# Optimization experiments

Hardware: AMD Instinct MI355X
Metric: run time of the kernel (lower is better)

## Reference

```python
import jax, jax.numpy as jnp
import numpy as np

INPUT_DIM = 1024
HIDDEN_DIM = 1024
NUM_HEADS = 16
HEAD_DIM = HIDDEN_DIM // NUM_HEADS


def setup_inputs() -> dict:
    key = jax.random.key(0)
    ks = jax.random.split(key, 11)
    B, S = 2, 2048
    s_in = 1.0 / np.sqrt(INPUT_DIM)
    s_hid = 1.0 / np.sqrt(HIDDEN_DIM)
    return {
        "query": jax.random.normal(ks[0], (B, S, INPUT_DIM), jnp.float32),
        "key": jax.random.normal(ks[1], (B, S, INPUT_DIM), jnp.float32),
        "value": jax.random.normal(ks[2], (B, S, INPUT_DIM), jnp.float32),
        "Wq": jax.random.normal(ks[3], (INPUT_DIM, HIDDEN_DIM), jnp.float32) * s_in,
        "bq": jnp.zeros((HIDDEN_DIM,), jnp.float32),
        "Wk": jax.random.normal(ks[4], (INPUT_DIM, HEAD_DIM), jnp.float32) * s_in,
        "bk": jnp.zeros((HEAD_DIM,), jnp.float32),
        "Wv": jax.random.normal(ks[5], (INPUT_DIM, HEAD_DIM), jnp.float32) * s_in,
        "bv": jnp.zeros((HEAD_DIM,), jnp.float32),
        "Wo": jax.random.normal(ks[6], (HIDDEN_DIM, INPUT_DIM), jnp.float32) * s_hid,
        "bo": jnp.zeros((INPUT_DIM,), jnp.float32),
    }


def reference(query, key, value, Wq, bq, Wk, bk, Wv, bv, Wo, bo):
    B, S, _ = query.shape
    # projections
    q = query @ Wq + bq                       # [B,S,H*D]
    k = key @ Wk + bk                         # [B,S,D]  (single shared head)
    v = value @ Wv + bv                       # [B,S,D]
    q = q.reshape(B, S, NUM_HEADS, HEAD_DIM)  # [B,S,H,D]
    # MQA scores: shared K broadcast over query heads
    scores = jnp.einsum('bqhd,bkd->bhqk', q, k) / np.sqrt(HIDDEN_DIM)
    attn = jax.nn.softmax(scores, axis=-1)    # [B,H,Q,K]
    out = jnp.einsum('bhqk,bkd->bqhd', attn, v)  # [B,Q,H,D]
    out = out.reshape(B, S, HIDDEN_DIM)
    return out @ Wo + bo
```

## Files before the change

### kernel.cpp

```cpp
#include <hip/hip_runtime.h>


typedef unsigned int   u32;
typedef unsigned short u16;
typedef union { float4 v; float f[4]; } f4u;
typedef __attribute__((ext_vector_type(8)))  short frag16;
typedef __attribute__((ext_vector_type(4)))  float f32x4;
typedef __attribute__((ext_vector_type(16))) float f32x16;
typedef union { frag16 v; u32 w[4]; u16 e[8]; } bf8u;

static __device__ __forceinline__ u16 f2bf(float x) {
  union { float f; u32 u; } v; v.f = x;
  u32 r = v.u + 0x7fff + ((v.u >> 16) & 1);
  return (u16)(r >> 16);
}

static __device__ __forceinline__ u32 cvt_pk_bf16(float lo, float hi) {
  u32 r;
  asm("v_cvt_pk_bf16_f32 %0, %1, %2" : "=v"(r) : "v"(lo), "v"(hi));
  return r;
}

static __device__ void tcvt_tile(const float* __restrict__ src,
                                 u16* __restrict__ dst,
                                 int C, int ldT, int rt, int ct,
                                 float (*t)[65]) {
  const int r0 = rt * 64, c0 = ct * 64;
  const int tr  = threadIdx.x >> 4;
  const int tc4 = (threadIdx.x & 15) * 4;
#pragma unroll
  for (int i = 0; i < 4; ++i) {
    f4u v; v.v = *(const float4*)(src + (size_t)(r0 + tr + i * 16) * C + c0 + tc4);
    t[tr + i * 16][tc4 + 0] = v.f[0];
    t[tr + i * 16][tc4 + 1] = v.f[1];
    t[tr + i * 16][tc4 + 2] = v.f[2];
    t[tr + i * 16][tc4 + 3] = v.f[3];
  }
  __syncthreads();
#pragma unroll
  for (int i = 0; i < 4; ++i) {
    const int oc = tr + i * 16;
    ushort4 o;
    o.x = f2bf(t[tc4 + 0][oc]);
    o.y = f2bf(t[tc4 + 1][oc]);
    o.z = f2bf(t[tc4 + 2][oc]);
    o.w = f2bf(t[tc4 + 3][oc]);
    *(ushort4*)(dst + (size_t)(c0 + oc) * ldT + r0 + tc4) = o;
  }
}

__global__ __launch_bounds__(256)
void prep_w(const float* __restrict__ Wq, const float* __restrict__ Wo,
            const float* __restrict__ Wk, const float* __restrict__ Wv,
            u16* __restrict__ wq_t, u16* __restrict__ wo_t,
            u16* __restrict__ wk_t, u16* __restrict__ wv_t) {
  __shared__ float t[64][65];
  const int bid = blockIdx.x;
  if (bid < 256)      tcvt_tile(Wq, wq_t, 1024, 1024, bid >> 4, bid & 15, t);
  else if (bid < 512) tcvt_tile(Wo, wo_t, 1024, 1024, (bid - 256) >> 4, (bid - 256) & 15, t);
  else if (bid < 528) tcvt_tile(Wk, wk_t, 64, 1024, bid - 512, 0, t);
  else                tcvt_tile(Wv, wv_t, 64, 1024, bid - 528, 0, t);
}

#define GP 72
template <bool A_FP32>
static __device__ void gemm64(const float* __restrict__ Af32,
                              const u16* __restrict__ Abf,
                              const u16* __restrict__ Bt,
                              const float* __restrict__ bias,
                              void* __restrict__ Cout, int out_mode,
                              float oscale,
                              int row0, int col0, int N, int K, int ldT,
                              u16* As, u16* Bs) {
  const int tid  = threadIdx.x;
  const int lane = tid & 63;
  const int quad = lane >> 4, l15 = lane & 15;
  const int w = tid >> 6, wy = w >> 1, wx = w & 1;

  f32x4 acc[2][2];
#pragma unroll
  for (int i = 0; i < 2; ++i)
#pragma unroll
    for (int j = 0; j < 2; ++j) {
      acc[i][j][0] = 0.f; acc[i][j][1] = 0.f;
      acc[i][j][2] = 0.f; acc[i][j][3] = 0.f;
    }

  const int r = tid >> 2, c16 = (tid & 3) * 16;

  for (int k0 = 0; k0 < K; k0 += 64) {
    frag16 a0, a1;
    if (A_FP32) {
      const float* ap = Af32 + (size_t)(row0 + r) * K + k0 + c16;
      f4u x0, x1, x2, x3;
      x0.v = *(const float4*)(ap);
      x1.v = *(const float4*)(ap + 4);
      x2.v = *(const float4*)(ap + 8);
      x3.v = *(const float4*)(ap + 12);
      bf8u t0, t1;
      t0.w[0] = cvt_pk_bf16(x0.f[0], x0.f[1]);
      t0.w[1] = cvt_pk_bf16(x0.f[2], x0.f[3]);
      t0.w[2] = cvt_pk_bf16(x1.f[0], x1.f[1]);
      t0.w[3] = cvt_pk_bf16(x1.f[2], x1.f[3]);
      t1.w[0] = cvt_pk_bf16(x2.f[0], x2.f[1]);
      t1.w[1] = cvt_pk_bf16(x2.f[2], x2.f[3]);
      t1.w[2] = cvt_pk_bf16(x3.f[0], x3.f[1]);
      t1.w[3] = cvt_pk_bf16(x3.f[2], x3.f[3]);
      a0 = t0.v; a1 = t1.v;
    } else {
      const u16* ap = Abf + (size_t)(row0 + r) * K + k0 + c16;
      a0 = *(const frag16*)(ap);
      a1 = *(const frag16*)(ap + 8);
    }
    const u16* bp = Bt + (size_t)(col0 + r) * K + k0 + c16;
    const frag16 b0 = *(const frag16*)(bp);
    const frag16 b1 = *(const frag16*)(bp + 8);
    __syncthreads();
    *(frag16*)(&As[r * GP + c16])     = a0;
    *(frag16*)(&As[r * GP + c16 + 8]) = a1;
    *(frag16*)(&Bs[r * GP + c16])     = b0;
    *(frag16*)(&Bs[r * GP + c16 + 8]) = b1;
    __syncthreads();
#pragma unroll
    for (int ks = 0; ks < 2; ++ks) {
      frag16 af[2], bf[2];
#pragma unroll
      for (int i = 0; i < 2; ++i)
        af[i] = *(const frag16*)(&As[(wy * 32 + i * 16 + l15) * GP + ks * 32 + quad * 8]);
#pragma unroll
      for (int j = 0; j < 2; ++j)
        bf[j] = *(const frag16*)(&Bs[(wx * 32 + j * 16 + l15) * GP + ks * 32 + quad * 8]);
#pragma unroll
      for (int i = 0; i < 2; ++i)
#pragma unroll
        for (int j = 0; j < 2; ++j)
          acc[i][j] = __builtin_amdgcn_mfma_f32_16x16x32_bf16(af[i], bf[j], acc[i][j], 0, 0, 0);
    }
  }

  float bj[2];
#pragma unroll
  for (int j = 0; j < 2; ++j)
    bj[j] = bias[col0 + wx * 32 + j * 16 + l15];

#pragma unroll
  for (int i = 0; i < 2; ++i) {
#pragma unroll
    for (int rr = 0; rr < 4; ++rr) {
      const size_t row = row0 + wy * 32 + i * 16 + quad * 4 + rr;
#pragma unroll
      for (int j = 0; j < 2; ++j) {
        const float v = (acc[i][j][rr] + bj[j]) * oscale;
        const int col = col0 + wx * 32 + j * 16 + l15;
        if (out_mode == 0)      ((float*)Cout)[row * N + col] = v;
        else if (out_mode == 1) ((u16*)Cout)[row * N + col] = f2bf(v);
        else                    ((u16*)Cout)[(size_t)col * ldT + row] = f2bf(v);
      }
    }
  }
}

#define C2_SCALE 0.045084220027780106f

__global__ __launch_bounds__(256, 4)
void proj(const float* __restrict__ query, const float* __restrict__ key,
          const float* __restrict__ value,
          const u16* __restrict__ wq_t, const u16* __restrict__ wk_t,
          const u16* __restrict__ wv_t,
          const float* __restrict__ bq, const float* __restrict__ bk,
          const float* __restrict__ bv,
          u16* __restrict__ q_bf, u16* __restrict__ k_bf,
          u16* __restrict__ vt_bf, int M, int K) {
  __shared__ __align__(16) u16 As[64 * GP];
  __shared__ __align__(16) u16 Bs[64 * GP];
  const int bid = blockIdx.x;
  if (bid < 64)
    gemm64<true>(key, nullptr, wk_t, bk, k_bf, 1, 1.0f, bid * 64, 0, 64, K, 0, As, Bs);
  else if (bid < 128)
    gemm64<true>(value, nullptr, wv_t, bv, vt_bf, 2, 1.0f, (bid - 64) * 64, 0, 64, K, M, As, Bs);
  else {
    const int q = bid - 128;
    gemm64<true>(query, nullptr, wq_t, bq, q_bf, 1, C2_SCALE,
                 (q >> 4) * 64, (q & 15) * 64, 1024, K, 0, As, Bs);
  }
}

__global__ __launch_bounds__(256, 4)
void out_proj(const u16* __restrict__ ao, const u16* __restrict__ wo_t,
              const float* __restrict__ bo, float* __restrict__ out,
              int M, int K) {
  __shared__ __align__(16) u16 As[64 * GP];
  __shared__ __align__(16) u16 Bs[64 * GP];
  gemm64<false>(nullptr, ao, wo_t, bo, out, 0, 1.0f,
                blockIdx.y * 64, blockIdx.x * 64, 1024, K, 0, As, Bs);
}

#define APITCH 72

__global__ __launch_bounds__(256, 4)
void mqa_flash_mfma(const u16* __restrict__ Qb,
                    const u16* __restrict__ Kb,
                    const u16* __restrict__ Vt,
                    u16* __restrict__ O) {
  const int S = 2048, HID = 1024, D = 64, BS = 4096;
  __shared__ u16 Ks[64 * APITCH];
  __shared__ u16 Vs[64 * APITCH];
  __shared__ u16 Ps[64 * APITCH];
  __shared__ float red[2][64];

  const int tid  = threadIdx.x;
  const int lane = tid & 63;
  const int w    = tid >> 6;
  const int l31  = lane & 31;
  const int hh   = lane >> 5;
  const int kh   = w & 1;
  const int qh   = w >> 1;
  const int qb = blockIdx.x, h = blockIdx.y, b = blockIdx.z;

  const int sr = tid >> 3;
  const int sc = (tid & 7) * 8;

  const u16* qrow = Qb + (size_t)(b * S + qb * 64 + qh * 32 + l31) * HID + h * D;
  frag16 qf[4];
#pragma unroll
  for (int ks = 0; ks < 4; ++ks)
    qf[ks] = *(const frag16*)(qrow + ks * 16 + hh * 8);

  f32x16 zero16;
#pragma unroll
  for (int r = 0; r < 16; ++r) zero16[r] = 0.f;

  f32x16 o_acc;
#pragma unroll
  for (int r = 0; r < 16; ++r) o_acc[r] = 0.f;
  float l_lane = 0.f;

  const u16* kbase = Kb + (size_t)(b * S) * D;
  const u16* vbase = Vt + (size_t)(b * S);

  frag16 pk0 = *(const frag16*)(kbase + (size_t)sr * D + sc);
  frag16 pk1 = *(const frag16*)(kbase + (size_t)(sr + 32) * D + sc);
  frag16 pv0 = *(const frag16*)(vbase + (size_t)sr * BS + sc);
  frag16 pv1 = *(const frag16*)(vbase + (size_t)(sr + 32) * BS + sc);
  *(frag16*)(&Ks[sr * APITCH + sc])        = pk0;
  *(frag16*)(&Ks[(sr + 32) * APITCH + sc]) = pk1;
  *(frag16*)(&Vs[sr * APITCH + sc])        = pv0;
  *(frag16*)(&Vs[(sr + 32) * APITCH + sc]) = pv1;
  __syncthreads();

  for (int kc = 0; kc < S; kc += 64) {
    const int nc = (kc + 64 < S) ? kc + 64 : kc;
    pk0 = *(const frag16*)(kbase + (size_t)(nc + sr) * D + sc);
    pk1 = *(const frag16*)(kbase + (size_t)(nc + sr + 32) * D + sc);
    pv0 = *(const frag16*)(vbase + (size_t)sr * BS + nc + sc);
    pv1 = *(const frag16*)(vbase + (size_t)(sr + 32) * BS + nc + sc);

    frag16 vf[4];
#pragma unroll
    for (int ks = 0; ks < 4; ++ks)
      vf[ks] = *(const frag16*)(&Vs[(kh * 32 + l31) * APITCH + ks * 16 + hh * 8]);

    f32x16 sa;
#pragma unroll
    for (int ks = 0; ks < 4; ++ks) {
      const frag16 kf = *(const frag16*)(&Ks[(kh * 32 + l31) * APITCH + ks * 16 + hh * 8]);
      sa = __builtin_amdgcn_mfma_f32_32x32x16_bf16(kf, qf[ks], ks ? sa : zero16, 0, 0, 0);
    }

    const int qrow_l = qh * 32 + l31;
    u16* prow = &Ps[qrow_l * APITCH + kh * 32];
#pragma unroll
    for (int g = 0; g < 4; ++g) {
      const float p0 = __builtin_amdgcn_exp2f(sa[g * 4 + 0]);
      const float p1 = __builtin_amdgcn_exp2f(sa[g * 4 + 1]);
      const float p2 = __builtin_amdgcn_exp2f(sa[g * 4 + 2]);
      const float p3 = __builtin_amdgcn_exp2f(sa[g * 4 + 3]);
      l_lane += (p0 + p1) + (p2 + p3);
      uint2 pk;
      pk.x = cvt_pk_bf16(p0, p1);
      pk.y = cvt_pk_bf16(p2, p3);
      *(uint2*)(&prow[g * 8 + hh * 4]) = pk;
    }
    __syncthreads();

#pragma unroll
    for (int ks = 0; ks < 4; ++ks) {
      const frag16 pf = *(const frag16*)(&Ps[(qh * 32 + l31) * APITCH + ks * 16 + hh * 8]);
      o_acc = __builtin_amdgcn_mfma_f32_32x32x16_bf16(pf, vf[ks], o_acc, 0, 0, 0);
    }

    *(frag16*)(&Ks[sr * APITCH + sc])        = pk0;
    *(frag16*)(&Ks[(sr + 32) * APITCH + sc]) = pk1;
    *(frag16*)(&Vs[sr * APITCH + sc])        = pv0;
    *(frag16*)(&Vs[(sr + 32) * APITCH + sc]) = pv1;
    __syncthreads();
  }

  l_lane += __shfl_xor(l_lane, 32);
  __syncthreads();
  if (lane < 32) red[kh][qh * 32 + l31] = l_lane;
  __syncthreads();

#pragma unroll
  for (int r = 0; r < 16; ++r) {
    const int q_local = qh * 32 + (r & 3) + 8 * (r >> 2) + 4 * hh;
    const float li = 1.f / (red[0][q_local] + red[1][q_local]);
    u16* orow = O + (size_t)(b * S + qb * 64 + q_local) * HID + h * D;
    orow[kh * 32 + l31] = f2bf(o_acc[r] * li);
  }
}

extern "C" void kernel_launch(void* const* d_in, const int* in_sizes, int n_in,
                              void* d_out, int out_size, void* d_ws, size_t ws_size,
                              hipStream_t stream) {
  const float* query = (const float*)d_in[0];
  const float* key   = (const float*)d_in[1];
  const float* value = (const float*)d_in[2];
  const float* Wq    = (const float*)d_in[3];
  const float* bq    = (const float*)d_in[4];
  const float* Wk    = (const float*)d_in[5];
  const float* bk    = (const float*)d_in[6];
  const float* Wv    = (const float*)d_in[7];
  const float* bv    = (const float*)d_in[8];
  const float* Wo    = (const float*)d_in[9];
  const float* bo    = (const float*)d_in[10];
  float* out = (float*)d_out;

  const int B = 2, S = 2048, IN = 1024, HID = 1024, H = 16, D = 64;
  const int M = B * S;
  const size_t MB = 1024 * 1024;

  char* ws = (char*)d_ws;
  u16* q_bf  = (u16*)ws;
  u16* ao_bf = (u16*)(ws + 8 * MB);
  u16* k_bf  = (u16*)(ws + 16 * MB);
  u16* vt_bf = (u16*)(ws + 16 * MB + 512 * 1024);
  u16* wq_t  = (u16*)(ws + 17 * MB);
  u16* wo_t  = (u16*)(ws + 19 * MB);
  u16* wk_t  = (u16*)(ws + 21 * MB);
  u16* wv_t  = (u16*)(ws + 21 * MB + 128 * 1024);

  dim3 blk(256);
  prep_w<<<dim3(544), blk, 0, stream>>>(Wq, Wo, Wk, Wv, wq_t, wo_t, wk_t, wv_t);
  proj<<<dim3(1152), blk, 0, stream>>>(query, key, value, wq_t, wk_t, wv_t,
                                       bq, bk, bv, q_bf, k_bf, vt_bf, M, IN);
  mqa_flash_mfma<<<dim3(S / 64, H, B), blk, 0, stream>>>(q_bf, k_bf, vt_bf, ao_bf);
  out_proj<<<dim3(HID / 64, M / 64), blk, 0, stream>>>(ao_bf, wo_t, bo, out, M, HID);
}
```

Baseline: 216.5 us.

## Use 128x128 bf16 GEMM tiles with direct global-to-LDS loads for Q and output projections

Pre-converts the fp32 query activations to bf16 inside the weight-prep kernel, reusing the attention-output buffer as scratch. The Q projection and the output projection then run through a new 128x128 tile GEMM whose operands are staged with global_load_lds. The larger tiles cut redundant global reads and per-tile overhead, and the direct loads skip the register staging step. In exchange there is an extra pass over the query tensor, fewer blocks in the grid, higher register and LDS use per block, and unpadded LDS rows that may cause bank conflicts.

```diff
diff --git a/kernel.cpp b/kernel.cpp
--- a/kernel.cpp
+++ b/kernel.cpp
@@ -19,6 +19,12 @@
   u32 r;
   asm("v_cvt_pk_bf16_f32 %0, %1, %2" : "=v"(r) : "v"(lo), "v"(hi));
   return r;
+}
+
+static __device__ __forceinline__ void gload_lds16(const u16* g, u16* l) {
+  __builtin_amdgcn_global_load_lds(
+      (const __attribute__((address_space(1))) u32*)g,
+      (__attribute__((address_space(3))) u32*)l, 16, 0, 0);
 }
 
 static __device__ void tcvt_tile(const float* __restrict__ src,
@@ -52,14 +58,107 @@
 __global__ __launch_bounds__(256)
 void prep_w(const float* __restrict__ Wq, const float* __restrict__ Wo,
             const float* __restrict__ Wk, const float* __restrict__ Wv,
+            const float* __restrict__ query,
             u16* __restrict__ wq_t, u16* __restrict__ wo_t,
-            u16* __restrict__ wk_t, u16* __restrict__ wv_t) {
+            u16* __restrict__ wk_t, u16* __restrict__ wv_t,
+            u16* __restrict__ xq_bf) {
+  const int bid = blockIdx.x;
+  if (bid >= 544) {
+    const size_t base = (size_t)(bid - 544) * 4096 + threadIdx.x * 16;
+    f4u x0, x1, x2, x3;
+    x0.v = *(const float4*)(query + base);
+    x1.v = *(const float4*)(query + base + 4);
+    x2.v = *(const float4*)(query + base + 8);
+    x3.v = *(const float4*)(query + base + 12);
+    bf8u t0, t1;
+    t0.w[0] = cvt_pk_bf16(x0.f[0], x0.f[1]);
+    t0.w[1] = cvt_pk_bf16(x0.f[2], x0.f[3]);
+    t0.w[2] = cvt_pk_bf16(x1.f[0], x1.f[1]);
+    t0.w[3] = cvt_pk_bf16(x1.f[2], x1.f[3]);
+    t1.w[0] = cvt_pk_bf16(x2.f[0], x2.f[1]);
+    t1.w[1] = cvt_pk_bf16(x2.f[2], x2.f[3]);
+    t1.w[2] = cvt_pk_bf16(x3.f[0], x3.f[1]);
+    t1.w[3] = cvt_pk_bf16(x3.f[2], x3.f[3]);
+    *(frag16*)(xq_bf + base)     = t0.v;
+    *(frag16*)(xq_bf + base + 8) = t1.v;
+    return;
+  }
   __shared__ float t[64][65];
-  const int bid = blockIdx.x;
   if (bid < 256)      tcvt_tile(Wq, wq_t, 1024, 1024, bid >> 4, bid & 15, t);
   else if (bid < 512) tcvt_tile(Wo, wo_t, 1024, 1024, (bid - 256) >> 4, (bid - 256) & 15, t);
   else if (bid < 528) tcvt_tile(Wk, wk_t, 64, 1024, bid - 512, 0, t);
   else                tcvt_tile(Wv, wv_t, 64, 1024, bid - 528, 0, t);
+}
+
+static __device__ void gemm128(const u16* __restrict__ Abf,
+                               const u16* __restrict__ Bt,
+                               const float* __restrict__ bias,
+                               void* __restrict__ Cout, int out_mode,
+                               float oscale, int row0, int col0,
+                               int N, int K, u16* As, u16* Bs) {
+  const int tid  = threadIdx.x;
+  const int lane = tid & 63;
+  const int quad = lane >> 4, l15 = lane & 15;
+  const int w = tid >> 6, wy = w >> 1, wx = w & 1;
+  const int lrow = lane >> 3, lcol = (lane & 7) * 8;
+
+  f32x4 acc[4][4];
+#pragma unroll
+  for (int i = 0; i < 4; ++i)
+#pragma unroll
+    for (int j = 0; j < 4; ++j) {
+      acc[i][j][0] = 0.f; acc[i][j][1] = 0.f;
+      acc[i][j][2] = 0.f; acc[i][j][3] = 0.f;
+    }
+
+  const u16* ag = Abf + (size_t)(row0 + w * 32 + lrow) * K + lcol;
+  const u16* bg = Bt  + (size_t)(col0 + w * 32 + lrow) * K + lcol;
+  u16* alds = As + w * 4 * 512;
+  u16* blds = Bs + w * 4 * 512;
+
+  for (int k0 = 0; k0 < K; k0 += 64) {
+    __syncthreads();
+#pragma unroll
+    for (int i = 0; i < 4; ++i) {
+      gload_lds16(ag + (size_t)i * 8 * K + k0, alds + i * 512);
+      gload_lds16(bg + (size_t)i * 8 * K + k0, blds + i * 512);
+    }
+    __syncthreads();
+#pragma unroll
+    for (int ks = 0; ks < 2; ++ks) {
+      frag16 af[4], bfr[4];
+#pragma unroll
+      for (int i = 0; i < 4; ++i)
+        af[i] = *(const frag16*)(&As[(wy * 64 + i * 16 + l15) * 64 + ks * 32 + quad * 8]);
+#pragma unroll
+      for (int j = 0; j < 4; ++j)
+        bfr[j] = *(const frag16*)(&Bs[(wx * 64 + j * 16 + l15) * 64 + ks * 32 + quad * 8]);
+#pragma unroll
+      for (int i = 0; i < 4; ++i)
+#pragma unroll
+        for (int j = 0; j < 4; ++j)
+          acc[i][j] = __builtin_amdgcn_mfma_f32_16x16x32_bf16(af[i], bfr[j], acc[i][j], 0, 0, 0);
+    }
+  }
+
+  float bj[4];
+#pragma unroll
+  for (int j = 0; j < 4; ++j)
+    bj[j] = bias[col0 + wx * 64 + j * 16 + l15];
+
+#pragma unroll
+  for (int i = 0; i < 4; ++i)
+#pragma unroll
+    for (int rr = 0; rr < 4; ++rr) {
+      const size_t row = row0 + wy * 64 + i * 16 + quad * 4 + rr;
+#pragma unroll
+      for (int j = 0; j < 4; ++j) {
+        const float v = (acc[i][j][rr] + bj[j]) * oscale;
+        const int col = col0 + wx * 64 + j * 16 + l15;
+        if (out_mode == 0) ((float*)Cout)[row * N + col] = v;
+        else               ((u16*)Cout)[row * N + col] = f2bf(v);
+      }
+    }
 }
 
 #define GP 72
@@ -162,37 +261,36 @@
 
 #define C2_SCALE 0.045084220027780106f
 
-__global__ __launch_bounds__(256, 4)
-void proj(const float* __restrict__ query, const float* __restrict__ key,
-          const float* __restrict__ value,
-          const u16* __restrict__ wq_t, const u16* __restrict__ wk_t,
-          const u16* __restrict__ wv_t,
-          const float* __restrict__ bq, const float* __restrict__ bk,
-          const float* __restrict__ bv,
-          u16* __restrict__ q_bf, u16* __restrict__ k_bf,
-          u16* __restrict__ vt_bf, int M, int K) {
-  __shared__ __align__(16) u16 As[64 * GP];
-  __shared__ __align__(16) u16 Bs[64 * GP];
+__global__ __launch_bounds__(256, 3)
+void proj2(const float* __restrict__ key, const float* __restrict__ value,
+           const u16* __restrict__ xq_bf,
+           const u16* __restrict__ wq_t, const u16* __restrict__ wk_t,
+           const u16* __restrict__ wv_t,
+           const float* __restrict__ bq, const float* __restrict__ bk,
+           const float* __restrict__ bv,
+           u16* __restrict__ q_bf, u16* __restrict__ k_bf,
+           u16* __restrict__ vt_bf, int M, int K) {
+  __shared__ __align__(16) u16 smem[16384];
   const int bid = blockIdx.x;
-  if (bid < 64)
-    gemm64<true>(key, nullptr, wk_t, bk, k_bf, 1, 1.0f, bid * 64, 0, 64, K, 0, As, Bs);
-  else if (bid < 128)
-    gemm64<true>(value, nullptr, wv_t, bv, vt_bf, 2, 1.0f, (bid - 64) * 64, 0, 64, K, M, As, Bs);
-  else {
-    const int q = bid - 128;
-    gemm64<true>(query, nullptr, wq_t, bq, q_bf, 1, C2_SCALE,
-                 (q >> 4) * 64, (q & 15) * 64, 1024, K, 0, As, Bs);
-  }
-}
-
-__global__ __launch_bounds__(256, 4)
+  if (bid < 256)
+    gemm128(xq_bf, wq_t, bq, q_bf, 1, C2_SCALE,
+            (bid >> 3) * 128, (bid & 7) * 128, 1024, K, smem, smem + 8192);
+  else if (bid < 320)
+    gemm64<true>(key, nullptr, wk_t, bk, k_bf, 1, 1.0f,
+                 (bid - 256) * 64, 0, 64, K, 0, smem, smem + 64 * GP);
+  else
+    gemm64<true>(value, nullptr, wv_t, bv, vt_bf, 2, 1.0f,
+                 (bid - 320) * 64, 0, 64, K, M, smem, smem + 64 * GP);
+}
+
+__global__ __launch_bounds__(256, 3)
 void out_proj(const u16* __restrict__ ao, const u16* __restrict__ wo_t,
               const float* __restrict__ bo, float* __restrict__ out,
               int M, int K) {
-  __shared__ __align__(16) u16 As[64 * GP];
-  __shared__ __align__(16) u16 Bs[64 * GP];
-  gemm64<false>(nullptr, ao, wo_t, bo, out, 0, 1.0f,
-                blockIdx.y * 64, blockIdx.x * 64, 1024, K, 0, As, Bs);
+  __shared__ __align__(16) u16 smem[16384];
+  const int bid = blockIdx.x;
+  gemm128(ao, wo_t, bo, out, 0, 1.0f,
+          (bid >> 3) * 128, (bid & 7) * 128, 1024, K, smem, smem + 8192);
 }
 
 #define APITCH 72
@@ -333,6 +431,7 @@
   char* ws = (char*)d_ws;
   u16* q_bf  = (u16*)ws;
   u16* ao_bf = (u16*)(ws + 8 * MB);
+  u16* xq_bf = ao_bf;
   u16* k_bf  = (u16*)(ws + 16 * MB);
   u16* vt_bf = (u16*)(ws + 16 * MB + 512 * 1024);
   u16* wq_t  = (u16*)(ws + 17 * MB);
@@ -341,9 +440,10 @@
   u16* wv_t  = (u16*)(ws + 21 * MB + 128 * 1024);
 
   dim3 blk(256);
-  prep_w<<<dim3(544), blk, 0, stream>>>(Wq, Wo, Wk, Wv, wq_t, wo_t, wk_t, wv_t);
-  proj<<<dim3(1152), blk, 0, stream>>>(query, key, value, wq_t, wk_t, wv_t,
+  prep_w<<<dim3(1568), blk, 0, stream>>>(Wq, Wo, Wk, Wv, query,
+                                         wq_t, wo_t, wk_t, wv_t, xq_bf);
+  proj2<<<dim3(384), blk, 0, stream>>>(key, value, xq_bf, wq_t, wk_t, wv_t,
                                        bq, bk, bv, q_bf, k_bf, vt_bf, M, IN);
   mqa_flash_mfma<<<dim3(S / 64, H, B), blk, 0, stream>>>(q_bf, k_bf, vt_bf, ao_bf);
-  out_proj<<<dim3(HID / 64, M / 64), blk, 0, stream>>>(ao_bf, wo_t, bo, out, M, HID);
-}
+  out_proj<<<dim3(256), blk, 0, stream>>>(ao_bf, wo_t, bo, out, M, HID);
+}
```

Measured after the change: 208.8 us. 3.6% less time.
